# Kernel tuning notes

Hardware: AMD Instinct MI355X
Metric: run time of the kernel (lower is better)

The kernel has to match this reference:

```python
import jax, jax.numpy as jnp
import numpy as np
import math

NUM_HEADS = 8
HEAD_SIZE = 64
ROPE_THETA = 10000.0


def _rope_cache(seq_len, dtype):
    # inv_freq: (head_size/2,)
    inv_freq = 1.0 / (ROPE_THETA ** (jnp.arange(0, HEAD_SIZE, 2, dtype=jnp.float32) / HEAD_SIZE))
    pos = jnp.arange(seq_len, dtype=jnp.float32)
    freqs = jnp.outer(pos, inv_freq)                      # (S, hd/2)
    cos = jnp.repeat(jnp.cos(freqs), 2, axis=-1)          # (S, hd) repeat_interleave(2)
    sin = jnp.repeat(jnp.sin(freqs), 2, axis=-1)
    return cos.astype(dtype), sin.astype(dtype)


def _rotate_half(x):
    # [x1, x2] -> [-x2, x1] (half-split, as in source)
    x1, x2 = jnp.split(x, 2, axis=-1)
    return jnp.concatenate((-x2, x1), axis=-1)


def setup_inputs() -> dict:
    key = jax.random.key(0)
    ks = jax.random.split(key, 8)
    B, S, H = 2, 4096, 512
    sc = 0.02
    return {
        'hidden_states': jax.random.normal(ks[0], (B, S, H), jnp.float32),
        'attention_mask': jnp.zeros((B, 1, 1, S), jnp.float32),
        'Wq': jax.random.normal(ks[1], (H, H), jnp.float32) * sc,
        'bq': jax.random.normal(ks[2], (H,), jnp.float32) * sc,
        'Wk': jax.random.normal(ks[3], (H, H), jnp.float32) * sc,
        'bk': jax.random.normal(ks[4], (H,), jnp.float32) * sc,
        'Wv': jax.random.normal(ks[5], (H, H), jnp.float32) * sc,
        'bv': jax.random.normal(ks[6], (H,), jnp.float32) * sc,
    }


def reference(hidden_states, attention_mask, Wq, bq, Wk, bk, Wv, bv):
    B, S, H = hidden_states.shape
    nh, hd = NUM_HEADS, HEAD_SIZE

    def proj(W, b):
        y = jnp.einsum('bsh,hd->bsd', hidden_states, W) + b
        return y.reshape(B, S, nh, hd).transpose(0, 2, 1, 3)  # (B, nh, S, hd)

    q = proj(Wq, bq)
    k = proj(Wk, bk)
    v = proj(Wv, bv)

    cos, sin = _rope_cache(S, hidden_states.dtype)  # (S, hd)
    cos = cos[None, None]
    sin = sin[None, None]
    q = q * cos + _rotate_half(q) * sin
    k = k * cos + _rotate_half(k) * sin

    scores = jnp.einsum('bhqd,bhkd->bhqk', q, k) / math.sqrt(hd)
    scores = scores + attention_mask
    probs = jax.nn.softmax(scores, axis=-1)  # dropout is identity at eval
    ctx = jnp.einsum('bhqk,bhkd->bhqd', probs, v)
    ctx = ctx.transpose(0, 2, 1, 3).reshape(B, S, nh * hd)
    return ctx
```

## Files before the change

### kernel.cpp

```cpp
#include <hip/hip_runtime.h>
#include <hip/hip_bf16.h>
#include <math.h>

typedef __bf16 bf16_t;
typedef bf16_t bf16x8 __attribute__((ext_vector_type(8)));
typedef bf16_t bf16x2 __attribute__((ext_vector_type(2)));
typedef float f32x2 __attribute__((ext_vector_type(2)));
typedef float f32x4 __attribute__((ext_vector_type(4)));
typedef float f32x16 __attribute__((ext_vector_type(16)));
typedef unsigned short u16;
typedef unsigned int u32;
typedef u32 u32x2 __attribute__((ext_vector_type(2)));
typedef u32 u32x4 __attribute__((ext_vector_type(4)));

#define AS1 __attribute__((address_space(1)))
#define AS3 __attribute__((address_space(3)))

#define LOG2E 1.4426950408889634f

static __device__ __forceinline__ void gll16(const void* g, void* l){
  __builtin_amdgcn_global_load_lds((const AS1 u32*)g, (AS3 u32*)l, 16, 0, 0);
}

static __device__ __forceinline__ u16 f2bf(float f){
  u32 u = __builtin_bit_cast(u32, f);
  u = u + 0x7FFFu + ((u >> 16) & 1u);
  return (u16)(u >> 16);
}

static __device__ __forceinline__ u32 pk2(float a, float b){
  f32x2 v = {a, b};
  bf16x2 w = __builtin_convertvector(v, bf16x2);
  return __builtin_bit_cast(u32, w);
}

static __device__ __forceinline__ float ex2(float x){
#if __has_builtin(__builtin_amdgcn_exp2f)
  return __builtin_amdgcn_exp2f(x);
#else
  return __expf(0.6931471805599453f * x);
#endif
}

static __device__ __forceinline__ void swap32(u32& a, u32& b, int hi){
#if __has_builtin(__builtin_amdgcn_permlane32_swap)
  auto r = __builtin_amdgcn_permlane32_swap((int)a, (int)b, false, false);
  a = (u32)r[0];
  b = (u32)r[1];
#else
  u32 xa = (u32)__shfl_xor((int)a, 32);
  u32 xb = (u32)__shfl_xor((int)b, 32);
  u32 na = hi ? xb : a;
  u32 nb = hi ? b : xa;
  a = na; b = nb;
#endif
}

__global__ void k_cast_hidden(const float* __restrict__ h, u16* __restrict__ hb, int n4){
  int i = blockIdx.x * blockDim.x + threadIdx.x;
  int stride = gridDim.x * blockDim.x;
  for (; i < n4; i += stride){
    float4 v = ((const float4*)h)[i];
    ushort4 o;
    o.x = f2bf(v.x); o.y = f2bf(v.y); o.z = f2bf(v.z); o.w = f2bf(v.w);
    ((ushort4*)hb)[i] = o;
  }
}

__global__ __launch_bounds__(256) void k_rope(float* __restrict__ cs){
  int idx = blockIdx.x * 256 + threadIdx.x;
  int s = idx >> 5, i = idx & 31;
  double invf = 1.0 / pow(10000.0, (double)(2 * i) / 64.0);
  float ang = (float)s * (float)invf;
  float sn, cv;
  sincosf(ang, &sn, &cv);
  f32x4 v = {cv, sn, cv, sn};
  *(f32x4*)&cs[(size_t)s * 128 + i * 4] = v;
}

__global__ __launch_bounds__(256) void k_prep_w(const float* __restrict__ Wq, const float* __restrict__ Wk,
                         const float* __restrict__ Wv, const float* __restrict__ bq,
                         const float* __restrict__ bk, const float* __restrict__ bv,
                         u16* __restrict__ wt, float* __restrict__ bc){
  __shared__ float T[64][65];
  int blk = blockIdx.x;
  int t = blk >> 6, rem = blk & 63;
  int tj = rem >> 3, tk = rem & 7;
  int j0 = tj * 64, k0 = tk * 64;
  const float* W = (t == 0) ? Wq : (t == 1 ? Wk : Wv);
  int tid = threadIdx.x;

#pragma unroll
  for (int it = 0; it < 4; ++it){
    int idx = it * 256 + tid;
    int r = idx >> 4, c4 = idx & 15;
    float4 v = *(const float4*)&W[(size_t)(k0 + r) * 512 + j0 + c4 * 4];
    T[r][c4 * 4 + 0] = v.x; T[r][c4 * 4 + 1] = v.y;
    T[r][c4 * 4 + 2] = v.z; T[r][c4 * 4 + 3] = v.w;
  }
  __syncthreads();

#pragma unroll
  for (int it = 0; it < 2; ++it){
    int idx = it * 256 + tid;
    int rr = idx >> 3, g8 = idx & 7;
    u32x4 wv;
#pragma unroll
    for (int e = 0; e < 4; ++e)
      wv[e] = pk2(T[g8 * 8 + 2 * e][rr], T[g8 * 8 + 2 * e + 1][rr]);
    *(u32x4*)&wt[(size_t)(t * 512 + j0 + rr) * 512 + k0 + g8 * 8] = wv;
  }

  int gi = blk * 256 + tid;
  if (gi < 1536){
    int tt = gi >> 9, jj = gi & 511;
    const float* bsrc = (tt == 0) ? bq : (tt == 1 ? bk : bv);
    bc[gi] = bsrc[jj];
  }
}

__global__ __launch_bounds__(256) void k_proj(const u16* __restrict__ hb, const u16* __restrict__ wt,
                      const float* __restrict__ bc, const float* __restrict__ cs,
                      u16* __restrict__ qws, u16* __restrict__ kws, u16* __restrict__ vt){
  __shared__ __align__(16) u16 SH[2][128 * 64];
  u16* At = SH[0];
  u16* Bt = SH[1];
  int tid = threadIdx.x;
  int lane = tid & 63;
  int c = lane & 15, g = lane >> 4;
  int wave = tid >> 6;
  int wm = wave >> 1, wn = wave & 1;
  int m0 = blockIdx.x * 128;
  int n0 = blockIdx.y * 128;

  const f32x4 vzero = {0.f, 0.f, 0.f, 0.f};
  f32x4 acc[4][4];
#pragma unroll
  for (int a = 0; a < 4; ++a)
#pragma unroll
    for (int b2 = 0; b2 < 4; ++b2) acc[a][b2] = vzero;

  for (int kc = 0; kc < 512; kc += 64){
    __syncthreads();
#pragma unroll
    for (int it = 0; it < 4; ++it){
      int j16 = it * 256 + tid;
      int row = j16 >> 3, u = j16 & 7;
      int us = u ^ (row & 7);
      gll16(hb + (size_t)(m0 + row) * 512 + kc + us * 8, &At[j16 * 8]);
      gll16(wt + (size_t)(n0 + row) * 512 + kc + us * 8, &Bt[j16 * 8]);
    }
    __syncthreads();
#pragma unroll
    for (int ch = 0; ch < 2; ++ch){
      bf16x8 af[4], bfg[4];
#pragma unroll
      for (int mt = 0; mt < 4; ++mt){
        int r = wm * 64 + mt * 16 + c;
        af[mt] = *(const bf16x8*)&At[r * 64 + ((g + 4 * ch) ^ (r & 7)) * 8];
      }
#pragma unroll
      for (int nt = 0; nt < 4; ++nt){
        int r = wn * 64 + nt * 16 + c;
        bfg[nt] = *(const bf16x8*)&Bt[r * 64 + ((g + 4 * ch) ^ (r & 7)) * 8];
      }
#pragma unroll
      for (int mt = 0; mt < 4; ++mt)
#pragma unroll
        for (int nt = 0; nt < 4; ++nt)
          acc[mt][nt] = __builtin_amdgcn_mfma_f32_16x16x32_bf16(af[mt], bfg[nt], acc[mt][nt], 0, 0, 0);
    }
  }

  int colbase = n0 + wn * 64;
  int typ = colbase >> 9;
  int head = (colbase >> 6) & 7;
  int rowbase = m0 + wm * 64;
  int bb = rowbase >> 12, s0 = rowbase & 4095;
  float bias[4];
#pragma unroll
  for (int nt = 0; nt < 4; ++nt) bias[nt] = bc[colbase + nt * 16 + c];

  if (typ == 2){
    __syncthreads();
    u16* Tw = &SH[0][0] + wave * 4096;
#pragma unroll
    for (int nt = 0; nt < 4; ++nt){
      int n = nt * 16 + c;
#pragma unroll
      for (int mt = 0; mt < 4; ++mt){
        float a0 = acc[mt][nt][0] + bias[nt];
        float a1 = acc[mt][nt][1] + bias[nt];
        float a2 = acc[mt][nt][2] + bias[nt];
        float a3 = acc[mt][nt][3] + bias[nt];
        int p = (mt * 4 + g) ^ (c & 14);
        u32x2 wv = { pk2(a0, a1), pk2(a2, a3) };
        *(u32x2*)&Tw[n * 64 + p * 4] = wv;
      }
    }
    __syncthreads();
    size_t vbase = (size_t)(bb * 8 + head) * 64 * 4096;
#pragma unroll
    for (int pass = 0; pass < 8; ++pass){
      int n = pass * 8 + (lane >> 3);
      int lu = (lane & 7) * 2;
      int p = lu ^ (n & 14);
      u32x4 vv = *(const u32x4*)&Tw[n * 64 + p * 4];
      *(u32x4*)&vt[vbase + (size_t)n * 4096 + s0 + (lane & 7) * 8] = vv;
    }
  } else {
    u16* dst = (typ == 0) ? qws : kws;
    float scale = (typ == 0) ? 0.125f : 1.0f;
#pragma unroll
    for (int mt = 0; mt < 4; ++mt){
#pragma unroll
      for (int reg = 0; reg < 4; ++reg){
        int m = rowbase + mt * 16 + g * 4 + reg;
        int b = m >> 12, s = m & 4095;
        const f32x2* cs_s = (const f32x2*)(cs + (size_t)s * 128);
        size_t base = ((size_t)(b * 8 + head) * 4096 + s) * 64;
#pragma unroll
        for (int nt = 0; nt < 4; ++nt){
          int nn = nt * 16 + c;
          float y = acc[mt][nt][reg] + bias[nt];
          f32x2 p2 = cs_s[nn];
          float rot;
          if (nn < 32){
            rot = -(acc[mt][nt + 2][reg] + bias[nt + 2]);
          } else {
            rot = acc[mt][nt - 2][reg] + bias[nt - 2];
          }
          float o = (y * p2[0] + rot * p2[1]) * scale;
          dst[base + nn] = f2bf(o);
        }
      }
    }
  }
}

template<int NSPLIT>
__global__ __launch_bounds__(256, 4) void k_attn(const u16* __restrict__ qws, const u16* __restrict__ kws,
                      const u16* __restrict__ vtws, const float* __restrict__ mask,
                      float* __restrict__ out, float* __restrict__ pctx, float* __restrict__ pml){
  __shared__ __align__(16) u16 smem[2][2][64 * 64];

  int tid = threadIdx.x;
  int lane = tid & 63;
  int q = lane & 31, hi = lane >> 5;
  int wave = tid >> 6;

  int cpx = (gridDim.x >> 3);
  int nbid = (blockIdx.x & 7) * cpx + (blockIdx.x >> 3);
  int slice = nbid / (32 * NSPLIT);
  int rem = nbid - slice * 32 * NSPLIT;
  int ksplit = rem >> 5;
  int qt = rem & 31;
  int b = slice >> 3, head = slice & 7;
  int q0 = qt * 128 + wave * 32;
  const int NT = 64 / NSPLIT;
  int kstart = ksplit * (4096 / NSPLIT);

  const u16* qs = qws + (size_t)slice * 4096 * 64;
  const u16* ks = kws + (size_t)slice * 4096 * 64;
  const u16* vs = vtws + (size_t)slice * 64 * 4096;
  const float* mk = mask + b * 4096;

  const u16* qrow = qs + (size_t)(q0 + q) * 64;
  bf16x8 qf[4];
#pragma unroll
  for (int dblk = 0; dblk < 4; ++dblk)
    qf[dblk] = *(const bf16x8*)&qrow[dblk * 16 + hi * 8];

  const f32x16 vz = {0.f,0.f,0.f,0.f,0.f,0.f,0.f,0.f,0.f,0.f,0.f,0.f,0.f,0.f,0.f,0.f};
  f32x16 ctx0 = vz, ctx1 = vz;
  float m_run = -1e30f, l_run = 0.f;
  float ml = m_run * LOG2E;

  auto stage = [&](int buf, int kc){
#pragma unroll
    for (int it = 0; it < 2; ++it){
      int j = it * 256 + tid;
      int row = j >> 3, u = j & 7;
      int us = u ^ (row & 7);
      gll16(ks + (size_t)(kc + row) * 64 + us * 8, &smem[buf][0][j * 8]);
      gll16(vs + (size_t)row * 4096 + kc + us * 8, &smem[buf][1][j * 8]);
    }
  };

  stage(0, kstart);

  for (int t = 0; t < NT; ++t){
    int kc = kstart + t * 64;
    __syncthreads();
    if (t < NT - 1) stage((t + 1) & 1, kc + 64);
    const u16* Kb  = &smem[t & 1][0][0];
    const u16* Vtc = &smem[t & 1][1][0];

    f32x16 sv[2];
    __builtin_amdgcn_s_setprio(1);
#pragma unroll
    for (int kb = 0; kb < 2; ++kb){
      f32x16 acc = vz;
#pragma unroll
      for (int dblk = 0; dblk < 4; ++dblk){
        int row = kb * 32 + q;
        bf16x8 kf = *(const bf16x8*)&Kb[row * 64 + (((dblk * 2 + hi) ^ (row & 7)) * 8)];
        acc = __builtin_amdgcn_mfma_f32_32x32x16_bf16(kf, qf[dblk], acc, 0, 0, 0);
      }
      sv[kb] = acc;
    }
    __builtin_amdgcn_s_setprio(0);
#pragma unroll
    for (int kb = 0; kb < 2; ++kb)
#pragma unroll
      for (int gg = 0; gg < 4; ++gg){
        float4 m4 = *(const float4*)&mk[kc + kb * 32 + gg * 8 + hi * 4];
        sv[kb][4 * gg + 0] += m4.x;
        sv[kb][4 * gg + 1] += m4.y;
        sv[kb][4 * gg + 2] += m4.z;
        sv[kb][4 * gg + 3] += m4.w;
      }

#define SVV(j) sv[(j) >> 4][(j) & 15]
    float tr[11];
#pragma unroll
    for (int i = 0; i < 10; ++i)
      tr[i] = fmaxf(fmaxf(SVV(3 * i), SVV(3 * i + 1)), SVV(3 * i + 2));
    tr[10] = fmaxf(SVV(30), SVV(31));
#undef SVV
    float u0 = fmaxf(fmaxf(tr[0], tr[1]), tr[2]);
    float u1 = fmaxf(fmaxf(tr[3], tr[4]), tr[5]);
    float u2 = fmaxf(fmaxf(tr[6], tr[7]), tr[8]);
    float u3 = fmaxf(tr[9], tr[10]);
    float pmax = fmaxf(fmaxf(fmaxf(u0, u1), u2), u3);
    pmax = fmaxf(pmax, __shfl_xor(pmax, 32));

    if (__any(pmax > m_run + 8.f)){
      float mnew = fmaxf(m_run, pmax);
      float al = ex2((m_run - mnew) * LOG2E);
      m_run = mnew;
      ml = mnew * LOG2E;
      l_run *= al;
#pragma unroll
      for (int r = 0; r < 16; ++r){ ctx0[r] *= al; ctx1[r] *= al; }
    }

    float rsp[4] = {0.f, 0.f, 0.f, 0.f};
#pragma unroll
    for (int kb = 0; kb < 2; ++kb)
#pragma unroll
      for (int r = 0; r < 16; ++r){
        float p = ex2(fmaf(sv[kb][r], LOG2E, -ml));
        sv[kb][r] = p;
        rsp[r & 3] += p;
      }
    float rs = (rsp[0] + rsp[1]) + (rsp[2] + rsp[3]);
    rs += __shfl_xor(rs, 32);
    l_run += rs;

    u32 W0[2][4], W1[2][4];
#pragma unroll
    for (int kb = 0; kb < 2; ++kb)
#pragma unroll
      for (int g = 0; g < 4; ++g){
        W0[kb][g] = pk2(sv[kb][4 * g + 0], sv[kb][4 * g + 1]);
        W1[kb][g] = pk2(sv[kb][4 * g + 2], sv[kb][4 * g + 3]);
      }

    bf16x8 pb[4];
#pragma unroll
    for (int kblk = 0; kblk < 4; ++kblk){
      int kb = kblk >> 1, j = kblk & 1;
      u32 w0 = W0[kb][2 * j + 0], w2 = W0[kb][2 * j + 1];
      u32 w1 = W1[kb][2 * j + 0], w3 = W1[kb][2 * j + 1];
      swap32(w0, w2, hi);
      swap32(w1, w3, hi);
      u32x4 wv = {w0, w1, w2, w3};
      pb[kblk] = __builtin_bit_cast(bf16x8, wv);
    }

    __builtin_amdgcn_s_setprio(1);
#pragma unroll
    for (int kblk = 0; kblk < 4; ++kblk){
      int row0 = q;
      bf16x8 vf0 = *(const bf16x8*)&Vtc[row0 * 64 + (((kblk * 2 + hi) ^ (row0 & 7)) * 8)];
      ctx0 = __builtin_amdgcn_mfma_f32_32x32x16_bf16(vf0, pb[kblk], ctx0, 0, 0, 0);
      int row1 = 32 + q;
      bf16x8 vf1 = *(const bf16x8*)&Vtc[row1 * 64 + (((kblk * 2 + hi) ^ (row1 & 7)) * 8)];
      ctx1 = __builtin_amdgcn_mfma_f32_32x32x16_bf16(vf1, pb[kblk], ctx1, 0, 0, 0);
    }
    __builtin_amdgcn_s_setprio(0);
  }

  if (NSPLIT == 1){
    float invl = 1.0f / l_run;
    float* orow = out + (size_t)(b * 4096 + q0 + q) * 512 + head * 64;
#pragma unroll
    for (int g = 0; g < 4; ++g){
      float4 o0, o1;
      o0.x = ctx0[4 * g + 0] * invl; o0.y = ctx0[4 * g + 1] * invl;
      o0.z = ctx0[4 * g + 2] * invl; o0.w = ctx0[4 * g + 3] * invl;
      *(float4*)&orow[8 * g + 4 * hi] = o0;
      o1.x = ctx1[4 * g + 0] * invl; o1.y = ctx1[4 * g + 1] * invl;
      o1.z = ctx1[4 * g + 2] * invl; o1.w = ctx1[4 * g + 3] * invl;
      *(float4*)&orow[32 + 8 * g + 4 * hi] = o1;
    }
  } else {
    size_t row = (size_t)ksplit * 65536 + slice * 4096 + q0 + q;
    float* prow = pctx + row * 64;
#pragma unroll
    for (int g = 0; g < 4; ++g){
      float4 o0, o1;
      o0.x = ctx0[4 * g + 0]; o0.y = ctx0[4 * g + 1];
      o0.z = ctx0[4 * g + 2]; o0.w = ctx0[4 * g + 3];
      *(float4*)&prow[8 * g + 4 * hi] = o0;
      o1.x = ctx1[4 * g + 0]; o1.y = ctx1[4 * g + 1];
      o1.z = ctx1[4 * g + 2]; o1.w = ctx1[4 * g + 3];
      *(float4*)&prow[32 + 8 * g + 4 * hi] = o1;
    }
    if (hi == 0){
      f32x2 mlv = {m_run, l_run};
      *(f32x2*)&pml[row * 2] = mlv;
    }
  }
}

__global__ __launch_bounds__(256) void k_merge(const float* __restrict__ pctx, const float* __restrict__ pml,
                                               float* __restrict__ out){
  int idx = blockIdx.x * 256 + threadIdx.x;
  int row = idx >> 4, dq = (idx & 15) * 4;
  f32x2 ml0 = *(const f32x2*)&pml[(size_t)row * 2];
  f32x2 ml1 = *(const f32x2*)&pml[((size_t)65536 + row) * 2];
  float ms = fmaxf(ml0[0], ml1[0]);
  float w0 = ex2((ml0[0] - ms) * LOG2E);
  float w1 = ex2((ml1[0] - ms) * LOG2E);
  float rdenom = 1.0f / (w0 * ml0[1] + w1 * ml1[1]);
  float4 c0 = *(const float4*)&pctx[(size_t)row * 64 + dq];
  float4 c1 = *(const float4*)&pctx[((size_t)65536 + row) * 64 + dq];
  float4 o;
  o.x = (w0 * c0.x + w1 * c1.x) * rdenom;
  o.y = (w0 * c0.y + w1 * c1.y) * rdenom;
  o.z = (w0 * c0.z + w1 * c1.z) * rdenom;
  o.w = (w0 * c0.w + w1 * c1.w) * rdenom;
  int slice = row >> 12, s = row & 4095;
  int b = slice >> 3, head = slice & 7;
  *(float4*)&out[(size_t)(b * 4096 + s) * 512 + head * 64 + dq] = o;
}

extern "C" void kernel_launch(void* const* d_in, const int* in_sizes, int n_in,
                              void* d_out, int out_size, void* d_ws, size_t ws_size,
                              hipStream_t stream) {
  const float* hidden = (const float*)d_in[0];
  const float* mask   = (const float*)d_in[1];
  const float* Wq = (const float*)d_in[2];
  const float* bq = (const float*)d_in[3];
  const float* Wk = (const float*)d_in[4];
  const float* bk = (const float*)d_in[5];
  const float* Wv = (const float*)d_in[6];
  const float* bv = (const float*)d_in[7];
  float* out = (float*)d_out;
  char* ws = (char*)d_ws;

  u16* hb    = (u16*)(ws + 0x00000000);
  u16* wt    = (u16*)(ws + 0x00900000);
  float* bc  = (float*)(ws + 0x00B00000);
  float* cs  = (float*)(ws + 0x00B10000);
  u16* qws   = (u16*)(ws + 0x00E00000);
  u16* kws   = (u16*)(ws + 0x01600000);
  u16* vtws  = (u16*)(ws + 0x01E00000);
  float* pctx= (float*)(ws + 0x02600000);
  float* pml = (float*)(ws + 0x04600000);

  bool split = ws_size >= 0x04700000ull;

  k_cast_hidden<<<dim3(2048), dim3(256), 0, stream>>>(hidden, hb, (2 * 4096 * 512) / 4);
  k_rope<<<dim3(512), dim3(256), 0, stream>>>(cs);
  k_prep_w<<<dim3(192), dim3(256), 0, stream>>>(Wq, Wk, Wv, bq, bk, bv, wt, bc);
  k_proj<<<dim3(64, 12), dim3(256), 0, stream>>>(hb, wt, bc, cs, qws, kws, vtws);
  if (split){
    k_attn<2><<<dim3(1024), dim3(256), 0, stream>>>(qws, kws, vtws, mask, out, pctx, pml);
    k_merge<<<dim3(4096), dim3(256), 0, stream>>>(pctx, pml, out);
  } else {
    k_attn<1><<<dim3(512), dim3(256), 0, stream>>>(qws, kws, vtws, mask, out, pctx, pml);
  }
}
```

Measured before the change: 160.8 us.

## Process 64 query rows per wave to reuse K/V fragments across two tiles

Each wave now handles two 32-row query tiles instead of one, so every K and V fragment read from LDS feeds two MFMAs, halving LDS traffic and barrier/staging overhead per unit of work. The block tile grows to 256 queries, the grid is halved, and launch bounds drop to 2 blocks per SM to make room for the doubled accumulators and score registers. The trade-off is fewer blocks (512 with split, about two per CU on a 256-CU part) and lower occupancy, which may hurt latency hiding and load balance.

```diff
diff --git a/kernel.cpp b/kernel.cpp
--- a/kernel.cpp
+++ b/kernel.cpp
@@ -239,7 +239,7 @@
 }
 
 template<int NSPLIT>
-__global__ __launch_bounds__(256, 4) void k_attn(const u16* __restrict__ qws, const u16* __restrict__ kws,
+__global__ __launch_bounds__(256, 2) void k_attn(const u16* __restrict__ qws, const u16* __restrict__ kws,
                       const u16* __restrict__ vtws, const float* __restrict__ mask,
                       float* __restrict__ out, float* __restrict__ pctx, float* __restrict__ pml){
   __shared__ __align__(16) u16 smem[2][2][64 * 64];
@@ -251,12 +251,12 @@
 
   int cpx = (gridDim.x >> 3);
   int nbid = (blockIdx.x & 7) * cpx + (blockIdx.x >> 3);
-  int slice = nbid / (32 * NSPLIT);
-  int rem = nbid - slice * 32 * NSPLIT;
-  int ksplit = rem >> 5;
-  int qt = rem & 31;
+  int slice = nbid / (16 * NSPLIT);
+  int rem = nbid - slice * 16 * NSPLIT;
+  int ksplit = rem >> 4;
+  int qt = rem & 15;
   int b = slice >> 3, head = slice & 7;
-  int q0 = qt * 128 + wave * 32;
+  int q0 = qt * 256 + wave * 64;
   const int NT = 64 / NSPLIT;
   int kstart = ksplit * (4096 / NSPLIT);
 
@@ -265,16 +265,21 @@
   const u16* vs = vtws + (size_t)slice * 64 * 4096;
   const float* mk = mask + b * 4096;
 
-  const u16* qrow = qs + (size_t)(q0 + q) * 64;
-  bf16x8 qf[4];
-#pragma unroll
-  for (int dblk = 0; dblk < 4; ++dblk)
-    qf[dblk] = *(const bf16x8*)&qrow[dblk * 16 + hi * 8];
+  bf16x8 qf[2][4];
+#pragma unroll
+  for (int h = 0; h < 2; ++h){
+    const u16* qrow = qs + (size_t)(q0 + h * 32 + q) * 64;
+#pragma unroll
+    for (int dblk = 0; dblk < 4; ++dblk)
+      qf[h][dblk] = *(const bf16x8*)&qrow[dblk * 16 + hi * 8];
+  }
 
   const f32x16 vz = {0.f,0.f,0.f,0.f,0.f,0.f,0.f,0.f,0.f,0.f,0.f,0.f,0.f,0.f,0.f,0.f};
-  f32x16 ctx0 = vz, ctx1 = vz;
-  float m_run = -1e30f, l_run = 0.f;
-  float ml = m_run * LOG2E;
+  f32x16 ctx[2][2];
+#pragma unroll
+  for (int h = 0; h < 2; ++h){ ctx[h][0] = vz; ctx[h][1] = vz; }
+  float m_run[2] = {-1e30f, -1e30f}, l_run[2] = {0.f, 0.f};
+  float ml[2] = {-1e30f * LOG2E, -1e30f * LOG2E};
 
   auto stage = [&](int buf, int kc){
 #pragma unroll
@@ -296,87 +301,97 @@
     const u16* Kb  = &smem[t & 1][0][0];
     const u16* Vtc = &smem[t & 1][1][0];
 
-    f32x16 sv[2];
+    f32x16 sv[2][2];
     __builtin_amdgcn_s_setprio(1);
 #pragma unroll
     for (int kb = 0; kb < 2; ++kb){
-      f32x16 acc = vz;
+      f32x16 a0 = vz, a1 = vz;
 #pragma unroll
       for (int dblk = 0; dblk < 4; ++dblk){
         int row = kb * 32 + q;
         bf16x8 kf = *(const bf16x8*)&Kb[row * 64 + (((dblk * 2 + hi) ^ (row & 7)) * 8)];
-        acc = __builtin_amdgcn_mfma_f32_32x32x16_bf16(kf, qf[dblk], acc, 0, 0, 0);
-      }
-      sv[kb] = acc;
+        a0 = __builtin_amdgcn_mfma_f32_32x32x16_bf16(kf, qf[0][dblk], a0, 0, 0, 0);
+        a1 = __builtin_amdgcn_mfma_f32_32x32x16_bf16(kf, qf[1][dblk], a1, 0, 0, 0);
+      }
+      sv[0][kb] = a0;
+      sv[1][kb] = a1;
     }
     __builtin_amdgcn_s_setprio(0);
-#pragma unroll
-    for (int kb = 0; kb < 2; ++kb)
+
+#pragma unroll
+    for (int kb = 0; kb < 2; ++kb){
+      f32x16 mv;
 #pragma unroll
       for (int gg = 0; gg < 4; ++gg){
         float4 m4 = *(const float4*)&mk[kc + kb * 32 + gg * 8 + hi * 4];
-        sv[kb][4 * gg + 0] += m4.x;
-        sv[kb][4 * gg + 1] += m4.y;
-        sv[kb][4 * gg + 2] += m4.z;
-        sv[kb][4 * gg + 3] += m4.w;
-      }
-
-#define SVV(j) sv[(j) >> 4][(j) & 15]
-    float tr[11];
-#pragma unroll
-    for (int i = 0; i < 10; ++i)
-      tr[i] = fmaxf(fmaxf(SVV(3 * i), SVV(3 * i + 1)), SVV(3 * i + 2));
-    tr[10] = fmaxf(SVV(30), SVV(31));
+        mv[4 * gg + 0] = m4.x; mv[4 * gg + 1] = m4.y;
+        mv[4 * gg + 2] = m4.z; mv[4 * gg + 3] = m4.w;
+      }
+      sv[0][kb] = sv[0][kb] + mv;
+      sv[1][kb] = sv[1][kb] + mv;
+    }
+
+#pragma unroll
+    for (int h = 0; h < 2; ++h){
+#define SVV(j) sv[h][(j) >> 4][(j) & 15]
+      float tr[11];
+#pragma unroll
+      for (int i = 0; i < 10; ++i)
+        tr[i] = fmaxf(fmaxf(SVV(3 * i), SVV(3 * i + 1)), SVV(3 * i + 2));
+      tr[10] = fmaxf(SVV(30), SVV(31));
 #undef SVV
-    float u0 = fmaxf(fmaxf(tr[0], tr[1]), tr[2]);
-    float u1 = fmaxf(fmaxf(tr[3], tr[4]), tr[5]);
-    float u2 = fmaxf(fmaxf(tr[6], tr[7]), tr[8]);
-    float u3 = fmaxf(tr[9], tr[10]);
-    float pmax = fmaxf(fmaxf(fmaxf(u0, u1), u2), u3);
-    pmax = fmaxf(pmax, __shfl_xor(pmax, 32));
-
-    if (__any(pmax > m_run + 8.f)){
-      float mnew = fmaxf(m_run, pmax);
-      float al = ex2((m_run - mnew) * LOG2E);
-      m_run = mnew;
-      ml = mnew * LOG2E;
-      l_run *= al;
-#pragma unroll
-      for (int r = 0; r < 16; ++r){ ctx0[r] *= al; ctx1[r] *= al; }
-    }
-
-    float rsp[4] = {0.f, 0.f, 0.f, 0.f};
-#pragma unroll
-    for (int kb = 0; kb < 2; ++kb)
-#pragma unroll
-      for (int r = 0; r < 16; ++r){
-        float p = ex2(fmaf(sv[kb][r], LOG2E, -ml));
-        sv[kb][r] = p;
-        rsp[r & 3] += p;
-      }
-    float rs = (rsp[0] + rsp[1]) + (rsp[2] + rsp[3]);
-    rs += __shfl_xor(rs, 32);
-    l_run += rs;
-
-    u32 W0[2][4], W1[2][4];
-#pragma unroll
-    for (int kb = 0; kb < 2; ++kb)
-#pragma unroll
-      for (int g = 0; g < 4; ++g){
-        W0[kb][g] = pk2(sv[kb][4 * g + 0], sv[kb][4 * g + 1]);
-        W1[kb][g] = pk2(sv[kb][4 * g + 2], sv[kb][4 * g + 3]);
-      }
-
-    bf16x8 pb[4];
-#pragma unroll
-    for (int kblk = 0; kblk < 4; ++kblk){
-      int kb = kblk >> 1, j = kblk & 1;
-      u32 w0 = W0[kb][2 * j + 0], w2 = W0[kb][2 * j + 1];
-      u32 w1 = W1[kb][2 * j + 0], w3 = W1[kb][2 * j + 1];
-      swap32(w0, w2, hi);
-      swap32(w1, w3, hi);
-      u32x4 wv = {w0, w1, w2, w3};
-      pb[kblk] = __builtin_bit_cast(bf16x8, wv);
+      float u0 = fmaxf(fmaxf(tr[0], tr[1]), tr[2]);
+      float u1 = fmaxf(fmaxf(tr[3], tr[4]), tr[5]);
+      float u2 = fmaxf(fmaxf(tr[6], tr[7]), tr[8]);
+      float u3 = fmaxf(tr[9], tr[10]);
+      float pmax = fmaxf(fmaxf(fmaxf(u0, u1), u2), u3);
+      pmax = fmaxf(pmax, __shfl_xor(pmax, 32));
+
+      if (__any(pmax > m_run[h] + 8.f)){
+        float mnew = fmaxf(m_run[h], pmax);
+        float al = ex2((m_run[h] - mnew) * LOG2E);
+        m_run[h] = mnew;
+        ml[h] = mnew * LOG2E;
+        l_run[h] *= al;
+#pragma unroll
+        for (int r = 0; r < 16; ++r){ ctx[h][0][r] *= al; ctx[h][1][r] *= al; }
+      }
+
+      float rsp[4] = {0.f, 0.f, 0.f, 0.f};
+#pragma unroll
+      for (int kb = 0; kb < 2; ++kb)
+#pragma unroll
+        for (int r = 0; r < 16; ++r){
+          float p = ex2(fmaf(sv[h][kb][r], LOG2E, -ml[h]));
+          sv[h][kb][r] = p;
+          rsp[r & 3] += p;
+        }
+      float rs = (rsp[0] + rsp[1]) + (rsp[2] + rsp[3]);
+      rs += __shfl_xor(rs, 32);
+      l_run[h] += rs;
+    }
+
+    bf16x8 pb[2][4];
+#pragma unroll
+    for (int h = 0; h < 2; ++h){
+      u32 W0[2][4], W1[2][4];
+#pragma unroll
+      for (int kb = 0; kb < 2; ++kb)
+#pragma unroll
+        for (int g = 0; g < 4; ++g){
+          W0[kb][g] = pk2(sv[h][kb][4 * g + 0], sv[h][kb][4 * g + 1]);
+          W1[kb][g] = pk2(sv[h][kb][4 * g + 2], sv[h][kb][4 * g + 3]);
+        }
+#pragma unroll
+      for (int kblk = 0; kblk < 4; ++kblk){
+        int kb = kblk >> 1, j = kblk & 1;
+        u32 w0 = W0[kb][2 * j + 0], w2 = W0[kb][2 * j + 1];
+        u32 w1 = W1[kb][2 * j + 0], w3 = W1[kb][2 * j + 1];
+        swap32(w0, w2, hi);
+        swap32(w1, w3, hi);
+        u32x4 wv = {w0, w1, w2, w3};
+        pb[h][kblk] = __builtin_bit_cast(bf16x8, wv);
+      }
     }
 
     __builtin_amdgcn_s_setprio(1);
@@ -384,43 +399,51 @@
     for (int kblk = 0; kblk < 4; ++kblk){
       int row0 = q;
       bf16x8 vf0 = *(const bf16x8*)&Vtc[row0 * 64 + (((kblk * 2 + hi) ^ (row0 & 7)) * 8)];
-      ctx0 = __builtin_amdgcn_mfma_f32_32x32x16_bf16(vf0, pb[kblk], ctx0, 0, 0, 0);
+      ctx[0][0] = __builtin_amdgcn_mfma_f32_32x32x16_bf16(vf0, pb[0][kblk], ctx[0][0], 0, 0, 0);
+      ctx[1][0] = __builtin_amdgcn_mfma_f32_32x32x16_bf16(vf0, pb[1][kblk], ctx[1][0], 0, 0, 0);
       int row1 = 32 + q;
       bf16x8 vf1 = *(const bf16x8*)&Vtc[row1 * 64 + (((kblk * 2 + hi) ^ (row1 & 7)) * 8)];
-      ctx1 = __builtin_amdgcn_mfma_f32_32x32x16_bf16(vf1, pb[kblk], ctx1, 0, 0, 0);
+      ctx[0][1] = __builtin_amdgcn_mfma_f32_32x32x16_bf16(vf1, pb[0][kblk], ctx[0][1], 0, 0, 0);
+      ctx[1][1] = __builtin_amdgcn_mfma_f32_32x32x16_bf16(vf1, pb[1][kblk], ctx[1][1], 0, 0, 0);
     }
     __builtin_amdgcn_s_setprio(0);
   }
 
   if (NSPLIT == 1){
-    float invl = 1.0f / l_run;
-    float* orow = out + (size_t)(b * 4096 + q0 + q) * 512 + head * 64;
-#pragma unroll
-    for (int g = 0; g < 4; ++g){
-      float4 o0, o1;
-      o0.x = ctx0[4 * g + 0] * invl; o0.y = ctx0[4 * g + 1] * invl;
-      o0.z = ctx0[4 * g + 2] * invl; o0.w = ctx0[4 * g + 3] * invl;
-      *(float4*)&orow[8 * g + 4 * hi] = o0;
-      o1.x = ctx1[4 * g + 0] * invl; o1.y = ctx1[4 * g + 1] * invl;
-      o1.z = ctx1[4 * g + 2] * invl; o1.w = ctx1[4 * g + 3] * invl;
-      *(float4*)&orow[32 + 8 * g + 4 * hi] = o1;
+#pragma unroll
+    for (int h = 0; h < 2; ++h){
+      float invl = 1.0f / l_run[h];
+      float* orow = out + (size_t)(b * 4096 + q0 + h * 32 + q) * 512 + head * 64;
+#pragma unroll
+      for (int g = 0; g < 4; ++g){
+        float4 o0, o1;
+        o0.x = ctx[h][0][4 * g + 0] * invl; o0.y = ctx[h][0][4 * g + 1] * invl;
+        o0.z = ctx[h][0][4 * g + 2] * invl; o0.w = ctx[h][0][4 * g + 3] * invl;
+        *(float4*)&orow[8 * g + 4 * hi] = o0;
+        o1.x = ctx[h][1][4 * g + 0] * invl; o1.y = ctx[h][1][4 * g + 1] * invl;
+        o1.z = ctx[h][1][4 * g + 2] * invl; o1.w = ctx[h][1][4 * g + 3] * invl;
+        *(float4*)&orow[32 + 8 * g + 4 * hi] = o1;
+      }
     }
   } else {
-    size_t row = (size_t)ksplit * 65536 + slice * 4096 + q0 + q;
-    float* prow = pctx + row * 64;
-#pragma unroll
-    for (int g = 0; g < 4; ++g){
-      float4 o0, o1;
-      o0.x = ctx0[4 * g + 0]; o0.y = ctx0[4 * g + 1];
-      o0.z = ctx0[4 * g + 2]; o0.w = ctx0[4 * g + 3];
-      *(float4*)&prow[8 * g + 4 * hi] = o0;
-      o1.x = ctx1[4 * g + 0]; o1.y = ctx1[4 * g + 1];
-      o1.z = ctx1[4 * g + 2]; o1.w = ctx1[4 * g + 3];
-      *(float4*)&prow[32 + 8 * g + 4 * hi] = o1;
-    }
-    if (hi == 0){
-      f32x2 mlv = {m_run, l_run};
-      *(f32x2*)&pml[row * 2] = mlv;
+#pragma unroll
+    for (int h = 0; h < 2; ++h){
+      size_t row = (size_t)ksplit * 65536 + slice * 4096 + q0 + h * 32 + q;
+      float* prow = pctx + row * 64;
+#pragma unroll
+      for (int g = 0; g < 4; ++g){
+        float4 o0, o1;
+        o0.x = ctx[h][0][4 * g + 0]; o0.y = ctx[h][0][4 * g + 1];
+        o0.z = ctx[h][0][4 * g + 2]; o0.w = ctx[h][0][4 * g + 3];
+        *(float4*)&prow[8 * g + 4 * hi] = o0;
+        o1.x = ctx[h][1][4 * g + 0]; o1.y = ctx[h][1][4 * g + 1];
+        o1.z = ctx[h][1][4 * g + 2]; o1.w = ctx[h][1][4 * g + 3];
+        *(float4*)&prow[32 + 8 * g + 4 * hi] = o1;
+      }
+      if (hi == 0){
+        f32x2 mlv = {m_run[h], l_run[h]};
+        *(f32x2*)&pml[row * 2] = mlv;
+      }
     }
   }
 }
@@ -478,9 +501,9 @@
   k_prep_w<<<dim3(192), dim3(256), 0, stream>>>(Wq, Wk, Wv, bq, bk, bv, wt, bc);
   k_proj<<<dim3(64, 12), dim3(256), 0, stream>>>(hb, wt, bc, cs, qws, kws, vtws);
   if (split){
-    k_attn<2><<<dim3(1024), dim3(256), 0, stream>>>(qws, kws, vtws, mask, out, pctx, pml);
+    k_attn<2><<<dim3(512), dim3(256), 0, stream>>>(qws, kws, vtws, mask, out, pctx, pml);
     k_merge<<<dim3(4096), dim3(256), 0, stream>>>(pctx, pml, out);
   } else {
-    k_attn<1><<<dim3(512), dim3(256), 0, stream>>>(qws, kws, vtws, mask, out, pctx, pml);
-  }
-}
+    k_attn<1><<<dim3(256), dim3(256), 0, stream>>>(qws, kws, vtws, mask, out, pctx, pml);
+  }
+}
```

Result: faster. 154.4 us (-4.0%).

## Fold log2e into Q, seed MFMA with mask, compute row sums via MFMA, split-K 4

Applied to the files above, without the earlier changes.

Pre-scales Q by log2e in the projection so scores come out in the log2 domain. The mask-minus-running-max term now seeds the QK MFMA accumulator, which removes the separate mask add and the per-element FMA before exp2. The softmax denominator is accumulated with an extra MFMA against a ones vector, replacing the VALU sum and cross-lane shuffle, and rescaling now triggers only when the max exceeds a fixed threshold. Attention is split 4 ways along K when workspace allows, with a templated merge, which adds more blocks and more partial-result traffic.

```diff
diff --git a/kernel.cpp b/kernel.cpp
--- a/kernel.cpp
+++ b/kernel.cpp
@@ -17,6 +17,7 @@
 #define AS3 __attribute__((address_space(3)))
 
 #define LOG2E 1.4426950408889634f
+#define THR_L2 11.541560327111707f
 
 static __device__ __forceinline__ void gll16(const void* g, void* l){
   __builtin_amdgcn_global_load_lds((const AS1 u32*)g, (AS3 u32*)l, 16, 0, 0);
@@ -210,7 +211,7 @@
     }
   } else {
     u16* dst = (typ == 0) ? qws : kws;
-    float scale = (typ == 0) ? 0.125f : 1.0f;
+    float scale = (typ == 0) ? 0.125f * LOG2E : 1.0f;
 #pragma unroll
     for (int mt = 0; mt < 4; ++mt){
 #pragma unroll
@@ -271,10 +272,13 @@
   for (int dblk = 0; dblk < 4; ++dblk)
     qf[dblk] = *(const bf16x8*)&qrow[dblk * 16 + hi * 8];
 
+  const u32x4 onesu = {0x3F803F80u, 0x3F803F80u, 0x3F803F80u, 0x3F803F80u};
+  const bf16x8 onesf = __builtin_bit_cast(bf16x8, onesu);
+
   const f32x16 vz = {0.f,0.f,0.f,0.f,0.f,0.f,0.f,0.f,0.f,0.f,0.f,0.f,0.f,0.f,0.f,0.f};
   f32x16 ctx0 = vz, ctx1 = vz;
-  float m_run = -1e30f, l_run = 0.f;
-  float ml = m_run * LOG2E;
+  f32x16 lacc = vz;
+  float ml = 0.f;
 
   auto stage = [&](int buf, int kc){
 #pragma unroll
@@ -300,26 +304,24 @@
     __builtin_amdgcn_s_setprio(1);
 #pragma unroll
     for (int kb = 0; kb < 2; ++kb){
-      f32x16 acc = vz;
+      f32x16 a;
+#pragma unroll
+      for (int gg = 0; gg < 4; ++gg){
+        float4 m4 = *(const float4*)&mk[kc + kb * 32 + gg * 8 + hi * 4];
+        a[4 * gg + 0] = fmaf(m4.x, LOG2E, -ml);
+        a[4 * gg + 1] = fmaf(m4.y, LOG2E, -ml);
+        a[4 * gg + 2] = fmaf(m4.z, LOG2E, -ml);
+        a[4 * gg + 3] = fmaf(m4.w, LOG2E, -ml);
+      }
 #pragma unroll
       for (int dblk = 0; dblk < 4; ++dblk){
         int row = kb * 32 + q;
         bf16x8 kf = *(const bf16x8*)&Kb[row * 64 + (((dblk * 2 + hi) ^ (row & 7)) * 8)];
-        acc = __builtin_amdgcn_mfma_f32_32x32x16_bf16(kf, qf[dblk], acc, 0, 0, 0);
-      }
-      sv[kb] = acc;
+        a = __builtin_amdgcn_mfma_f32_32x32x16_bf16(kf, qf[dblk], a, 0, 0, 0);
+      }
+      sv[kb] = a;
     }
     __builtin_amdgcn_s_setprio(0);
-#pragma unroll
-    for (int kb = 0; kb < 2; ++kb)
-#pragma unroll
-      for (int gg = 0; gg < 4; ++gg){
-        float4 m4 = *(const float4*)&mk[kc + kb * 32 + gg * 8 + hi * 4];
-        sv[kb][4 * gg + 0] += m4.x;
-        sv[kb][4 * gg + 1] += m4.y;
-        sv[kb][4 * gg + 2] += m4.z;
-        sv[kb][4 * gg + 3] += m4.w;
-      }
 
 #define SVV(j) sv[(j) >> 4][(j) & 15]
     float tr[11];
@@ -335,28 +337,24 @@
     float pmax = fmaxf(fmaxf(fmaxf(u0, u1), u2), u3);
     pmax = fmaxf(pmax, __shfl_xor(pmax, 32));
 
-    if (__any(pmax > m_run + 8.f)){
-      float mnew = fmaxf(m_run, pmax);
-      float al = ex2((m_run - mnew) * LOG2E);
-      m_run = mnew;
-      ml = mnew * LOG2E;
-      l_run *= al;
+    if (__any(pmax > THR_L2)){
+      float delta = fmaxf(pmax, 0.f);
+      ml += delta;
+      float al = ex2(-delta);
+      lacc[0] *= al;
 #pragma unroll
       for (int r = 0; r < 16; ++r){ ctx0[r] *= al; ctx1[r] *= al; }
-    }
-
-    float rsp[4] = {0.f, 0.f, 0.f, 0.f};
+#pragma unroll
+      for (int kb = 0; kb < 2; ++kb)
+#pragma unroll
+        for (int r = 0; r < 16; ++r) sv[kb][r] -= delta;
+    }
+
 #pragma unroll
     for (int kb = 0; kb < 2; ++kb)
 #pragma unroll
-      for (int r = 0; r < 16; ++r){
-        float p = ex2(fmaf(sv[kb][r], LOG2E, -ml));
-        sv[kb][r] = p;
-        rsp[r & 3] += p;
-      }
-    float rs = (rsp[0] + rsp[1]) + (rsp[2] + rsp[3]);
-    rs += __shfl_xor(rs, 32);
-    l_run += rs;
+      for (int r = 0; r < 16; ++r)
+        sv[kb][r] = ex2(sv[kb][r]);
 
     u32 W0[2][4], W1[2][4];
 #pragma unroll
@@ -388,12 +386,13 @@
       int row1 = 32 + q;
       bf16x8 vf1 = *(const bf16x8*)&Vtc[row1 * 64 + (((kblk * 2 + hi) ^ (row1 & 7)) * 8)];
       ctx1 = __builtin_amdgcn_mfma_f32_32x32x16_bf16(vf1, pb[kblk], ctx1, 0, 0, 0);
+      lacc = __builtin_amdgcn_mfma_f32_32x32x16_bf16(onesf, pb[kblk], lacc, 0, 0, 0);
     }
     __builtin_amdgcn_s_setprio(0);
   }
 
   if (NSPLIT == 1){
-    float invl = 1.0f / l_run;
+    float invl = 1.0f / lacc[0];
     float* orow = out + (size_t)(b * 4096 + q0 + q) * 512 + head * 64;
 #pragma unroll
     for (int g = 0; g < 4; ++g){
@@ -419,29 +418,40 @@
       *(float4*)&prow[32 + 8 * g + 4 * hi] = o1;
     }
     if (hi == 0){
-      f32x2 mlv = {m_run, l_run};
+      f32x2 mlv = {ml, lacc[0]};
       *(f32x2*)&pml[row * 2] = mlv;
     }
   }
 }
 
+template<int NSPLIT>
 __global__ __launch_bounds__(256) void k_merge(const float* __restrict__ pctx, const float* __restrict__ pml,
                                                float* __restrict__ out){
   int idx = blockIdx.x * 256 + threadIdx.x;
   int row = idx >> 4, dq = (idx & 15) * 4;
-  f32x2 ml0 = *(const f32x2*)&pml[(size_t)row * 2];
-  f32x2 ml1 = *(const f32x2*)&pml[((size_t)65536 + row) * 2];
-  float ms = fmaxf(ml0[0], ml1[0]);
-  float w0 = ex2((ml0[0] - ms) * LOG2E);
-  float w1 = ex2((ml1[0] - ms) * LOG2E);
-  float rdenom = 1.0f / (w0 * ml0[1] + w1 * ml1[1]);
-  float4 c0 = *(const float4*)&pctx[(size_t)row * 64 + dq];
-  float4 c1 = *(const float4*)&pctx[((size_t)65536 + row) * 64 + dq];
-  float4 o;
-  o.x = (w0 * c0.x + w1 * c1.x) * rdenom;
-  o.y = (w0 * c0.y + w1 * c1.y) * rdenom;
-  o.z = (w0 * c0.z + w1 * c1.z) * rdenom;
-  o.w = (w0 * c0.w + w1 * c1.w) * rdenom;
+  float mlv[NSPLIT], lv[NSPLIT], w[NSPLIT];
+  float ms = -3e38f;
+#pragma unroll
+  for (int i = 0; i < NSPLIT; ++i){
+    f32x2 t = *(const f32x2*)&pml[((size_t)i * 65536 + row) * 2];
+    mlv[i] = t[0]; lv[i] = t[1];
+    ms = fmaxf(ms, mlv[i]);
+  }
+  float den = 0.f;
+#pragma unroll
+  for (int i = 0; i < NSPLIT; ++i){
+    w[i] = ex2(mlv[i] - ms);
+    den += w[i] * lv[i];
+  }
+  float rden = 1.0f / den;
+  float4 o = {0.f, 0.f, 0.f, 0.f};
+#pragma unroll
+  for (int i = 0; i < NSPLIT; ++i){
+    float4 c = *(const float4*)&pctx[((size_t)i * 65536 + row) * 64 + dq];
+    o.x += w[i] * c.x; o.y += w[i] * c.y;
+    o.z += w[i] * c.z; o.w += w[i] * c.w;
+  }
+  o.x *= rden; o.y *= rden; o.z *= rden; o.w *= rden;
   int slice = row >> 12, s = row & 4095;
   int b = slice >> 3, head = slice & 7;
   *(float4*)&out[(size_t)(b * 4096 + s) * 512 + head * 64 + dq] = o;
@@ -469,18 +479,23 @@
   u16* kws   = (u16*)(ws + 0x01600000);
   u16* vtws  = (u16*)(ws + 0x01E00000);
   float* pctx= (float*)(ws + 0x02600000);
-  float* pml = (float*)(ws + 0x04600000);
-
-  bool split = ws_size >= 0x04700000ull;
 
   k_cast_hidden<<<dim3(2048), dim3(256), 0, stream>>>(hidden, hb, (2 * 4096 * 512) / 4);
   k_rope<<<dim3(512), dim3(256), 0, stream>>>(cs);
   k_prep_w<<<dim3(192), dim3(256), 0, stream>>>(Wq, Wk, Wv, bq, bk, bv, wt, bc);
   k_proj<<<dim3(64, 12), dim3(256), 0, stream>>>(hb, wt, bc, cs, qws, kws, vtws);
-  if (split){
+
+  size_t need4 = 0x02600000ull + 4ull * 0x01000000 + 4ull * 0x00080000;
+  size_t need2 = 0x02600000ull + 2ull * 0x01000000 + 2ull * 0x00080000;
+  if (ws_size >= need4){
+    float* pml = (float*)(ws + 0x02600000 + 4ull * 0x01000000);
+    k_attn<4><<<dim3(2048), dim3(256), 0, stream>>>(qws, kws, vtws, mask, out, pctx, pml);
+    k_merge<4><<<dim3(4096), dim3(256), 0, stream>>>(pctx, pml, out);
+  } else if (ws_size >= need2){
+    float* pml = (float*)(ws + 0x02600000 + 2ull * 0x01000000);
     k_attn<2><<<dim3(1024), dim3(256), 0, stream>>>(qws, kws, vtws, mask, out, pctx, pml);
-    k_merge<<<dim3(4096), dim3(256), 0, stream>>>(pctx, pml, out);
+    k_merge<2><<<dim3(4096), dim3(256), 0, stream>>>(pctx, pml, out);
   } else {
-    k_attn<1><<<dim3(512), dim3(256), 0, stream>>>(qws, kws, vtws, mask, out, pctx, pml);
-  }
-}
+    k_attn<1><<<dim3(512), dim3(256), 0, stream>>>(qws, kws, vtws, mask, out, (float*)ws, (float*)ws);
+  }
+}
```

Result: slower. 172.1 us (+7.0%).
